# Optimization experiments

Hardware: AMD Instinct MI355X
Metric: run time of the kernel (lower is better)

Reference implementation:

```python
import jax, jax.numpy as jnp
import numpy as np

D_EMBED = 512
NUM_HEADS = 8
HEAD_DIM = D_EMBED // NUM_HEADS
D_FF = 2048
B, L = 2, 4096
LN_EPS = 1e-5


def _layernorm(x, g, b):
    mu = jnp.mean(x, axis=-1, keepdims=True)
    var = jnp.mean(jnp.square(x - mu), axis=-1, keepdims=True)
    return (x - mu) * jax.lax.rsqrt(var + LN_EPS) * g + b


def setup_inputs() -> dict:
    key = jax.random.key(0)
    ks = jax.random.split(key, 16)
    s = 0.02
    inp = {
        "x": jax.random.normal(ks[0], (B, L, D_EMBED), dtype=jnp.float32),
        "mask": jnp.ones((B, 1, 1, L), dtype=jnp.int32),
        # attention projections (stored [in, out] for x @ W)
        "Wq": jax.random.normal(ks[1], (D_EMBED, D_EMBED), dtype=jnp.float32) * s,
        "bq": jnp.zeros((D_EMBED,), dtype=jnp.float32),
        "Wk": jax.random.normal(ks[2], (D_EMBED, D_EMBED), dtype=jnp.float32) * s,
        "bk": jnp.zeros((D_EMBED,), dtype=jnp.float32),
        "Wv": jax.random.normal(ks[3], (D_EMBED, D_EMBED), dtype=jnp.float32) * s,
        "bv": jnp.zeros((D_EMBED,), dtype=jnp.float32),
        "Wo": jax.random.normal(ks[4], (D_EMBED, D_EMBED), dtype=jnp.float32) * s,
        "bo": jnp.zeros((D_EMBED,), dtype=jnp.float32),
        # layernorms
        "ln1_g": jnp.ones((D_EMBED,), dtype=jnp.float32),
        "ln1_b": jnp.zeros((D_EMBED,), dtype=jnp.float32),
        "ln2_g": jnp.ones((D_EMBED,), dtype=jnp.float32),
        "ln2_b": jnp.zeros((D_EMBED,), dtype=jnp.float32),
        # FFN
        "W1": jax.random.normal(ks[5], (D_EMBED, D_FF), dtype=jnp.float32) * s,
        "b1": jnp.zeros((D_FF,), dtype=jnp.float32),
        "W2": jax.random.normal(ks[6], (D_FF, D_EMBED), dtype=jnp.float32) * s,
        "b2": jnp.zeros((D_EMBED,), dtype=jnp.float32),
    }
    return inp


def reference(x, mask, Wq, bq, Wk, bk, Wv, bv, Wo, bo, ln1_g, ln1_b,
              W1, b1, W2, b2, ln2_g, ln2_b):
    Bx, Lx, _ = x.shape
    # projections -> [B, H, L, Dh]
    def split_heads(t):
        return t.reshape(Bx, Lx, NUM_HEADS, HEAD_DIM).transpose(0, 2, 1, 3)
    q = split_heads(x @ Wq + bq)
    k = split_heads(x @ Wk + bk)
    v = split_heads(x @ Wv + bv)
    scores = jnp.einsum("bhqd,bhkd->bhqk", q, k) / jnp.sqrt(
        jnp.asarray(HEAD_DIM, dtype=x.dtype))
    scores = jnp.where(mask == 0, jnp.asarray(-1e9, dtype=x.dtype), scores)
    attn = jax.nn.softmax(scores, axis=-1)
    ctx = jnp.einsum("bhqk,bhkd->bhqd", attn, v)
    ctx = ctx.transpose(0, 2, 1, 3).reshape(Bx, Lx, D_EMBED)
    attn_out = ctx @ Wo + bo

    h = _layernorm(x + attn_out, ln1_g, ln1_b)
    ff = (jax.nn.gelu(h @ W1 + b1, approximate=False)) @ W2 + b2
    return _layernorm(h + ff, ln2_g, ln2_b)
```

## Files before the change

kernel.cpp:

```cpp
#include <hip/hip_runtime.h>
#include <hip/hip_bf16.h>
#include <math.h>

#define D_EMBED 512
#define NUM_HEADS 8
#define HEAD_DIM 64
#define D_FF 2048
#define BATCH 2
#define SEQ 4096
#define M_ROWS (BATCH*SEQ)
#define QSCALE 0.18033688011112042f

typedef __attribute__((ext_vector_type(8))) short short8;
typedef __attribute__((ext_vector_type(4))) short short4_t;
typedef __attribute__((ext_vector_type(4))) float f32x4;

#if __has_builtin(__builtin_amdgcn_mfma_f32_16x16x16bf16_1k)
#define MFMA_K16(a,b,c) __builtin_amdgcn_mfma_f32_16x16x16bf16_1k(a,b,c,0,0,0)
#elif __has_builtin(__builtin_amdgcn_mfma_f32_16x16x16_bf16)
#define MFMA_K16(a,b,c) __builtin_amdgcn_mfma_f32_16x16x16_bf16(a,b,c,0,0,0)
#else
#define MFMA_K16(a,b,c) (c)
#endif

#if __has_builtin(__builtin_amdgcn_exp2f)
#define EXP2(x) __builtin_amdgcn_exp2f(x)
#else
#define EXP2(x) exp2f(x)
#endif

__device__ inline unsigned short f2b(float f) {
    union { float f; unsigned u; } v; v.f = f;
    unsigned r = v.u + 0x7fffu + ((v.u >> 16) & 1u);
    return (unsigned short)(r >> 16);
}

__device__ inline float b2f(short s) {
    union { unsigned u; float f; } v;
    v.u = ((unsigned)(unsigned short)s) << 16;
    return v.f;
}

__device__ inline short4_t pk4(float p0, float p1, float p2, float p3) {
    union { __hip_bfloat162 h2[2]; short4_t s4; } u;
    u.h2[0] = __float22bfloat162_rn(make_float2(p0, p1));
    u.h2[1] = __float22bfloat162_rn(make_float2(p2, p3));
    return u.s4;
}

__device__ inline void gl2lds16(const void* g, void* l) {
    __builtin_amdgcn_global_load_lds(
        (const __attribute__((address_space(1))) unsigned int*)g,
        (__attribute__((address_space(3))) unsigned int*)l, 16, 0, 0);
}

template<int EPI>
__global__ __launch_bounds__(256) void gemm_bt(
    const unsigned short* __restrict__ A, const unsigned short* __restrict__ BT,
    const float* __restrict__ bias, void* __restrict__ Cout,
    int M, int N, int K)
{
    __shared__ __align__(16) unsigned short As[128*32];
    __shared__ __align__(16) unsigned short Bs[128*32];
    const int tid  = threadIdx.x;
    const int wave = tid >> 6, lane = tid & 63;
    const int wy = wave >> 1, wx = wave & 1;
    const int quad = lane >> 4, m16 = lane & 15;
    const int row0 = blockIdx.y * 128, n0 = blockIdx.x * 128;
    const int rdoff = (quad ^ ((m16 >> 1) & 3)) * 8;

    f32x4 acc[4][4];
#pragma unroll
    for (int i = 0; i < 4; i++)
#pragma unroll
        for (int j = 0; j < 4; j++) acc[i][j] = (f32x4){0.f,0.f,0.f,0.f};

    const int kIters = K >> 5;
    for (int kt = 0; kt < kIters; ++kt) {
        const int k0 = kt << 5;
#pragma unroll
        for (int it = 0; it < 2; ++it) {
            int g  = it*256 + tid;
            int r  = g >> 2;
            int c8 = (((g & 3) ^ ((g >> 3) & 3)) << 3);
            gl2lds16(A  + (size_t)(row0 + r)*K + k0 + c8, &As[(size_t)(it*256 + wave*64)*8]);
            gl2lds16(BT + (size_t)(n0  + r)*K + k0 + c8, &Bs[(size_t)(it*256 + wave*64)*8]);
        }
        __syncthreads();
        short8 a[4], b[4];
#pragma unroll
        for (int i = 0; i < 4; i++) a[i] = *(const short8*)&As[(wy*64 + i*16 + m16)*32 + rdoff];
#pragma unroll
        for (int j = 0; j < 4; j++) b[j] = *(const short8*)&Bs[(wx*64 + j*16 + m16)*32 + rdoff];
#pragma unroll
        for (int i = 0; i < 4; i++)
#pragma unroll
            for (int j = 0; j < 4; j++)
                acc[i][j] = __builtin_amdgcn_mfma_f32_16x16x32_bf16(a[i], b[j], acc[i][j], 0, 0, 0);
        __syncthreads();
    }

#pragma unroll
    for (int j = 0; j < 4; j++) {
        int col = n0 + wx*64 + j*16 + m16;
        float bj = bias[col];
#pragma unroll
        for (int i = 0; i < 4; i++) {
            int rbase = row0 + wy*64 + i*16 + quad*4;
#pragma unroll
            for (int r = 0; r < 4; r++) {
                float v = acc[i][j][r] + bj;
                size_t idx = (size_t)(rbase + r)*N + col;
                if (EPI == 0) {
                    ((unsigned short*)Cout)[idx] = f2b(v);
                } else {
                    float gv = 0.5f * v * (1.0f + erff(v * 0.70710678118654752f));
                    ((unsigned short*)Cout)[idx] = f2b(gv);
                }
            }
        }
    }
}

__global__ __launch_bounds__(256) void gemm_qkv(
    const unsigned short* __restrict__ A, const unsigned short* __restrict__ BT,
    const float* __restrict__ bias,
    unsigned short* __restrict__ Qp, unsigned short* __restrict__ Kp,
    unsigned short* __restrict__ Vp)
{
    const int K = 512;
    __shared__ __align__(16) unsigned short As[128*32];
    __shared__ __align__(16) unsigned short Bs[128*32];
    const int tid  = threadIdx.x;
    const int wave = tid >> 6, lane = tid & 63;
    const int wy = wave >> 1, wx = wave & 1;
    const int quad = lane >> 4, m16 = lane & 15;
    const int row0 = blockIdx.y * 128, n0 = blockIdx.x * 128;
    const int rdoff = (quad ^ ((m16 >> 1) & 3)) * 8;
    const int region = n0 >> 9;

    f32x4 acc[4][4];
#pragma unroll
    for (int i = 0; i < 4; i++)
#pragma unroll
        for (int j = 0; j < 4; j++) acc[i][j] = (f32x4){0.f,0.f,0.f,0.f};

    for (int kt = 0; kt < 16; ++kt) {
        const int k0 = kt << 5;
#pragma unroll
        for (int it = 0; it < 2; ++it) {
            int g  = it*256 + tid;
            int r  = g >> 2;
            int c8 = (((g & 3) ^ ((g >> 3) & 3)) << 3);
            gl2lds16(A  + (size_t)(row0 + r)*K + k0 + c8, &As[(size_t)(it*256 + wave*64)*8]);
            gl2lds16(BT + (size_t)(n0  + r)*K + k0 + c8, &Bs[(size_t)(it*256 + wave*64)*8]);
        }
        __syncthreads();
        short8 a[4], b[4];
#pragma unroll
        for (int i = 0; i < 4; i++) a[i] = *(const short8*)&As[(wy*64 + i*16 + m16)*32 + rdoff];
#pragma unroll
        for (int j = 0; j < 4; j++) b[j] = *(const short8*)&Bs[(wx*64 + j*16 + m16)*32 + rdoff];
#pragma unroll
        for (int i = 0; i < 4; i++)
#pragma unroll
            for (int j = 0; j < 4; j++)
                acc[i][j] = __builtin_amdgcn_mfma_f32_16x16x32_bf16(a[i], b[j], acc[i][j], 0, 0, 0);
        __syncthreads();
    }

    const float sc = (region == 0) ? QSCALE : 1.0f;
#pragma unroll
    for (int j = 0; j < 4; j++) {
        int col = n0 + wx*64 + j*16 + m16;
        float bj = bias[col];
        int cc = col & 511, h = cc >> 6, d = cc & 63;
#pragma unroll
        for (int i = 0; i < 4; i++) {
            int rbase = row0 + wy*64 + i*16 + quad*4;
#pragma unroll
            for (int r = 0; r < 4; r++) {
                float v = (acc[i][j][r] + bj) * sc;
                int row = rbase + r;
                int b = row >> 12, l = row & 4095;
                size_t bh = (size_t)(b*8 + h);
                if (region == 0) {
                    Qp[(bh*SEQ + l)*64 + d] = f2b(v);
                } else if (region == 1) {
                    Kp[(bh*SEQ + l)*64 + d] = f2b(v);
                } else {
                    int kt = l >> 7, kk = l & 127;
                    int qr = (kk >> 2) & 3, fi = (kk >> 4)*4 + (kk & 3);
                    Vp[((((bh*32 + kt)*4 + qr)*64 + d)*32) + fi] = f2b(v);
                }
            }
        }
    }
}

__global__ __launch_bounds__(256) void gemm_bt64(
    const unsigned short* __restrict__ A, const unsigned short* __restrict__ BT,
    const float* __restrict__ bias, unsigned short* __restrict__ Cout,
    int M, int N, int K)
{
    __shared__ __align__(16) unsigned short As[64*32];
    __shared__ __align__(16) unsigned short Bs[128*32];
    const int tid  = threadIdx.x;
    const int wave = tid >> 6, lane = tid & 63;
    const int wy = wave >> 1, wx = wave & 1;
    const int quad = lane >> 4, m16 = lane & 15;
    const int row0 = blockIdx.y * 64, n0 = blockIdx.x * 128;
    const int rdoff = (quad ^ ((m16 >> 1) & 3)) * 8;

    f32x4 acc[2][4];
#pragma unroll
    for (int i = 0; i < 2; i++)
#pragma unroll
        for (int j = 0; j < 4; j++) acc[i][j] = (f32x4){0.f,0.f,0.f,0.f};

    const int kIters = K >> 5;
    for (int kt = 0; kt < kIters; ++kt) {
        const int k0 = kt << 5;
        {
            int r = tid >> 2;
            int c8 = (((tid & 3) ^ ((tid >> 3) & 3)) << 3);
            gl2lds16(A + (size_t)(row0 + r)*K + k0 + c8, &As[(size_t)(wave*64)*8]);
        }
#pragma unroll
        for (int it = 0; it < 2; ++it) {
            int g  = it*256 + tid;
            int r  = g >> 2;
            int c8 = (((g & 3) ^ ((g >> 3) & 3)) << 3);
            gl2lds16(BT + (size_t)(n0 + r)*K + k0 + c8, &Bs[(size_t)(it*256 + wave*64)*8]);
        }
        __syncthreads();
        short8 a[2], b[4];
#pragma unroll
        for (int i = 0; i < 2; i++) a[i] = *(const short8*)&As[(wy*32 + i*16 + m16)*32 + rdoff];
#pragma unroll
        for (int j = 0; j < 4; j++) b[j] = *(const short8*)&Bs[(wx*64 + j*16 + m16)*32 + rdoff];
#pragma unroll
        for (int i = 0; i < 2; i++)
#pragma unroll
            for (int j = 0; j < 4; j++)
                acc[i][j] = __builtin_amdgcn_mfma_f32_16x16x32_bf16(a[i], b[j], acc[i][j], 0, 0, 0);
        __syncthreads();
    }

#pragma unroll
    for (int j = 0; j < 4; j++) {
        int col = n0 + wx*64 + j*16 + m16;
        float bj = bias[col];
#pragma unroll
        for (int i = 0; i < 2; i++) {
            int rbase = row0 + wy*32 + i*16 + quad*4;
#pragma unroll
            for (int r = 0; r < 4; r++) {
                float v = acc[i][j][r] + bj;
                Cout[(size_t)(rbase + r)*N + col] = f2b(v);
            }
        }
    }
}

__global__ __launch_bounds__(256) void prep(
    const float* __restrict__ Wq, const float* __restrict__ Wk,
    const float* __restrict__ Wv, const float* __restrict__ Wo,
    const float* __restrict__ W1, const float* __restrict__ W2,
    const float* __restrict__ bq, const float* __restrict__ bk,
    const float* __restrict__ bv, const int* __restrict__ mask,
    unsigned short* __restrict__ WqkvT, unsigned short* __restrict__ WoT,
    unsigned short* __restrict__ W1T, unsigned short* __restrict__ W2T,
    float* __restrict__ bqkv, int* __restrict__ mflag, unsigned* __restrict__ kmax2)
{
    const int id = blockIdx.x, t = threadIdx.x;
    if (id == 3072) {
        if (t < 64) {
            const int* m = mask + t*128;
            int all = 1;
            for (int i = 0; i < 128; i += 4) {
                int4 v = *(const int4*)(m + i);
                all &= (v.x && v.y && v.z && v.w) ? 1 : 0;
            }
            mflag[t] = all;
        }
        if (t < 16) kmax2[t] = 0u;
        for (int i = t; i < 1536; i += 256)
            bqkv[i] = (i < 512) ? bq[i] : ((i < 1024) ? bk[i-512] : bv[i-1024]);
        return;
    }
    __shared__ float tt[32][33];
    const float* W; unsigned short* WT; int K, N, bx, by;
    if (id < 256)       { W = Wq; WT = WqkvT;            K = 512;  N = 512;  bx = id & 15;  by = id >> 4; }
    else if (id < 512)  { int l = id - 256;  W = Wk; WT = WqkvT + 512*512;  K = 512;  N = 512;  bx = l & 15; by = l >> 4; }
    else if (id < 768)  { int l = id - 512;  W = Wv; WT = WqkvT + 1024*512; K = 512;  N = 512;  bx = l & 15; by = l >> 4; }
    else if (id < 1024) { int l = id - 768;  W = Wo; WT = WoT;              K = 512;  N = 512;  bx = l & 15; by = l >> 4; }
    else if (id < 2048) { int l = id - 1024; W = W1; WT = W1T;              K = 512;  N = 2048; bx = l & 63; by = l >> 6; }
    else                { int l = id - 2048; W = W2; WT = W2T;              K = 2048; N = 512;  bx = l & 15; by = l >> 4; }
    const int n0 = bx*32, k0 = by*32;
    const int x = t & 31, y = t >> 5;
#pragma unroll
    for (int yy = y; yy < 32; yy += 8) tt[yy][x] = W[(size_t)(k0+yy)*N + n0 + x];
    __syncthreads();
#pragma unroll
    for (int yy = y; yy < 32; yy += 8) WT[(size_t)(n0+yy)*K + k0 + x] = f2b(tt[x][yy]);
}

__global__ __launch_bounds__(256) void kmax_k(
    const unsigned short* __restrict__ Kp, unsigned* __restrict__ kmax2)
{
    const int bh = blockIdx.x, t = threadIdx.x;
    const int row = blockIdx.y*256 + t;
    const unsigned short* kp = Kp + ((size_t)bh*SEQ + row)*64;
    float s = 0.f;
#pragma unroll
    for (int c = 0; c < 8; ++c) {
        short8 v = *(const short8*)(kp + c*8);
#pragma unroll
        for (int j = 0; j < 8; ++j) { float f = b2f(v[j]); s += f*f; }
    }
#pragma unroll
    for (int off = 32; off >= 1; off >>= 1)
        s = fmaxf(s, __shfl_xor(s, off, 64));
    if ((t & 63) == 0) atomicMax(&kmax2[bh], __float_as_uint(s));
}

__global__ __launch_bounds__(256) void flash_attn(
    const unsigned short* __restrict__ Qp, const unsigned short* __restrict__ Kp,
    const unsigned short* __restrict__ Vp, const int* __restrict__ mask,
    const int* __restrict__ flags, const unsigned* __restrict__ kmax2,
    unsigned short* __restrict__ O)
{
    __shared__ __align__(16) unsigned short Ks[2][128*32];
    __shared__ __align__(16) unsigned short Vs[4][64*32];
    const int tid = threadIdx.x, wave = tid >> 6, lane = tid & 63;
    const int quad = lane >> 4, m16 = lane & 15;
    const int bh = blockIdx.y, b = bh >> 3, h = bh & 7;
    const int qbase = blockIdx.x * 64 + wave * 16;
    const int fsw = (m16 >> 1) & 3;
    const int koff = (quad ^ fsw) * 8;

    const unsigned short* Qb = Qp + (size_t)bh*SEQ*64;
    const unsigned short* Kb = Kp + (size_t)bh*SEQ*64;
    const unsigned short* Vb = Vp + (size_t)bh*32*4*64*32;
    const int* mbase = mask + b*SEQ;
    const int* fbase = flags + b*(SEQ/128);

    short8 qf[2];
    {
        const unsigned short* qp = Qb + (size_t)(qbase + m16)*64 + quad*8;
        qf[0] = *(const short8*)qp;
        qf[1] = *(const short8*)(qp + 32);
    }
    float qn2 = 0.f;
#pragma unroll
    for (int j = 0; j < 8; ++j) {
        float f0 = b2f(qf[0][j]), f1 = b2f(qf[1][j]);
        qn2 += f0*f0 + f1*f1;
    }
    qn2 += __shfl_xor(qn2, 16, 64);
    qn2 += __shfl_xor(qn2, 32, 64);
    const float M = sqrtf(qn2 * __uint_as_float(kmax2[bh]));
    const f32x4 cinit = (f32x4){-M, -M, -M, -M};

    f32x4 accO[4];
#pragma unroll
    for (int dj = 0; dj < 4; dj++) accO[dj] = (f32x4){0.f,0.f,0.f,0.f};
    float rs = 0.f;

    for (int kt = 0; kt < SEQ/128; ++kt) {
        const int key0 = kt * 128;
        const int allones = fbase[kt];
        __syncthreads();
#pragma unroll
        for (int it = 0; it < 2; ++it) {
            int g = it*256 + tid;
            int r = g >> 2;
            int c8 = (((g & 3) ^ ((g >> 3) & 3)) << 3);
            gl2lds16(Kb + (size_t)(key0 + r)*64 + c8,      &Ks[0][(it*256 + wave*64)*8]);
            gl2lds16(Kb + (size_t)(key0 + r)*64 + 32 + c8, &Ks[1][(it*256 + wave*64)*8]);
        }
        {
            int d = wave*16 + (lane >> 2), ch = lane & 3;
            int c8 = (ch ^ ((d >> 1) & 3)) * 8;
#pragma unroll
            for (int qr = 0; qr < 4; ++qr)
                gl2lds16(Vb + (((size_t)kt*4 + qr)*64 + d)*32 + c8,
                         &Vs[qr][wave*64*8]);
        }
        __syncthreads();

        short4_t pb[8];
#pragma unroll
        for (int nj = 0; nj < 8; ++nj) {
            short8 k0 = *(const short8*)&Ks[0][(nj*16 + m16)*32 + koff];
            short8 k1 = *(const short8*)&Ks[1][(nj*16 + m16)*32 + koff];
            f32x4 c = cinit;
            c = __builtin_amdgcn_mfma_f32_16x16x32_bf16(k0, qf[0], c, 0, 0, 0);
            c = __builtin_amdgcn_mfma_f32_16x16x32_bf16(k1, qf[1], c, 0, 0, 0);
            if (!allones) {
                int4 mv = *(const int4*)(mbase + key0 + nj*16 + quad*4);
                c[0] = mv.x ? c[0] : -1e9f;
                c[1] = mv.y ? c[1] : -1e9f;
                c[2] = mv.z ? c[2] : -1e9f;
                c[3] = mv.w ? c[3] : -1e9f;
            }
            float p0 = EXP2(c[0]);
            float p1 = EXP2(c[1]);
            float p2 = EXP2(c[2]);
            float p3 = EXP2(c[3]);
            rs += (p0 + p1) + (p2 + p3);
            pb[nj] = pk4(p0, p1, p2, p3);
        }

#pragma unroll
        for (int l = 0; l < 4; ++l) {
#pragma unroll
            for (int dj = 0; dj < 4; ++dj) {
                const unsigned short* vrow = &Vs[quad][(dj*16 + m16)*32 + ((l ^ fsw) * 8)];
                short4_t vlo = *(const short4_t*)vrow;
                short4_t vhi = *(const short4_t*)(vrow + 4);
                accO[dj] = MFMA_K16(vlo, pb[2*l],     accO[dj]);
                accO[dj] = MFMA_K16(vhi, pb[2*l + 1], accO[dj]);
            }
        }
    }

    rs += __shfl_xor(rs, 16, 64);
    rs += __shfl_xor(rs, 32, 64);
    float rl = 1.0f / rs;
#pragma unroll
    for (int dj = 0; dj < 4; ++dj) {
        short4_t o = pk4(accO[dj][0]*rl, accO[dj][1]*rl,
                         accO[dj][2]*rl, accO[dj][3]*rl);
        *(short4_t*)&O[(size_t)(b*SEQ + qbase + m16)*D_EMBED
                       + h*HEAD_DIM + dj*16 + quad*4] = o;
    }
}

__global__ __launch_bounds__(256) void ln_res1(
    const float* __restrict__ A, const unsigned short* __restrict__ Bv,
    const float* __restrict__ g, const float* __restrict__ be,
    unsigned short* __restrict__ Yb)
{
    const int wave = threadIdx.x >> 6, lane = threadIdx.x & 63;
    const int row = blockIdx.x * 4 + wave;
    const float* ap = A + (size_t)row*512 + lane*8;
    short8 bv = *(const short8*)(Bv + (size_t)row*512 + lane*8);
    float v[8]; float s = 0.f;
#pragma unroll
    for (int j = 0; j < 8; j++) { v[j] = ap[j] + b2f(bv[j]); s += v[j]; }
#pragma unroll
    for (int off = 32; off >= 1; off >>= 1) s += __shfl_xor(s, off, 64);
    float mu = s * (1.f/512.f);
    float q = 0.f;
#pragma unroll
    for (int j = 0; j < 8; j++) { v[j] -= mu; q += v[j]*v[j]; }
#pragma unroll
    for (int off = 32; off >= 1; off >>= 1) q += __shfl_xor(q, off, 64);
    float rstd = rsqrtf(q * (1.f/512.f) + 1e-5f);
#pragma unroll
    for (int j = 0; j < 8; j++) {
        float y = v[j]*rstd*g[lane*8+j] + be[lane*8+j];
        Yb[(size_t)row*512 + lane*8 + j] = f2b(y);
    }
}

__global__ __launch_bounds__(256) void ln_res2(
    const unsigned short* __restrict__ A, const unsigned short* __restrict__ Bv,
    const float* __restrict__ g, const float* __restrict__ be,
    float* __restrict__ Yf)
{
    const int wave = threadIdx.x >> 6, lane = threadIdx.x & 63;
    const int row = blockIdx.x * 4 + wave;
    short8 av = *(const short8*)(A  + (size_t)row*512 + lane*8);
    short8 bv = *(const short8*)(Bv + (size_t)row*512 + lane*8);
    float v[8]; float s = 0.f;
#pragma unroll
    for (int j = 0; j < 8; j++) { v[j] = b2f(av[j]) + b2f(bv[j]); s += v[j]; }
#pragma unroll
    for (int off = 32; off >= 1; off >>= 1) s += __shfl_xor(s, off, 64);
    float mu = s * (1.f/512.f);
    float q = 0.f;
#pragma unroll
    for (int j = 0; j < 8; j++) { v[j] -= mu; q += v[j]*v[j]; }
#pragma unroll
    for (int off = 32; off >= 1; off >>= 1) q += __shfl_xor(q, off, 64);
    float rstd = rsqrtf(q * (1.f/512.f) + 1e-5f);
#pragma unroll
    for (int j = 0; j < 8; j++) {
        float y = v[j]*rstd*g[lane*8+j] + be[lane*8+j];
        Yf[(size_t)row*512 + lane*8 + j] = y;
    }
}

__global__ __launch_bounds__(256) void cvt_f32_bf16(
    const float* __restrict__ X, unsigned short* __restrict__ Y, int n)
{
    int idx = (blockIdx.x * 256 + threadIdx.x) * 4;
    if (idx < n) {
        float4 v = *(const float4*)(X + idx);
        Y[idx+0] = f2b(v.x); Y[idx+1] = f2b(v.y);
        Y[idx+2] = f2b(v.z); Y[idx+3] = f2b(v.w);
    }
}

extern "C" void kernel_launch(void* const* d_in, const int* in_sizes, int n_in,
                              void* d_out, int out_size, void* d_ws, size_t ws_size,
                              hipStream_t stream)
{
    const float* x    = (const float*)d_in[0];
    const int*   mask = (const int*)  d_in[1];
    const float* Wq = (const float*)d_in[2];  const float* bq = (const float*)d_in[3];
    const float* Wk = (const float*)d_in[4];  const float* bk = (const float*)d_in[5];
    const float* Wv = (const float*)d_in[6];  const float* bv = (const float*)d_in[7];
    const float* Wo = (const float*)d_in[8];  const float* bo = (const float*)d_in[9];
    const float* ln1g = (const float*)d_in[10]; const float* ln1b = (const float*)d_in[11];
    const float* ln2g = (const float*)d_in[12]; const float* ln2b = (const float*)d_in[13];
    const float* W1 = (const float*)d_in[14]; const float* b1 = (const float*)d_in[15];
    const float* W2 = (const float*)d_in[16]; const float* b2 = (const float*)d_in[17];
    float* out = (float*)d_out;

    char* ws = (char*)d_ws;
    const size_t MB = 1024*1024;
    unsigned short* xb    = (unsigned short*)(ws + 0);
    unsigned short* WqkvT = (unsigned short*)(ws + 8*MB);
    unsigned short* W1T   = (unsigned short*)(ws + 10*MB);
    unsigned short* W2T   = (unsigned short*)(ws + 12*MB);
    unsigned short* WoT   = (unsigned short*)(ws + 14*MB);
    float*          bqkv  = (float*)(ws + 14*MB + 512*1024);
    int*            mflag = (int*)(ws + 14*MB + 768*1024);
    unsigned*       kmaxb = (unsigned*)(ws + 14*MB + 772*1024);
    unsigned short* Qp    = (unsigned short*)(ws + 15*MB);
    unsigned short* Kp    = (unsigned short*)(ws + 23*MB);
    unsigned short* Vp    = (unsigned short*)(ws + 31*MB);
    unsigned short* ctx   = (unsigned short*)(ws + 39*MB);
    unsigned short* atfb  = (unsigned short*)(ws + 47*MB);
    unsigned short* hb    = (unsigned short*)(ws + 0);
    unsigned short* Gb    = (unsigned short*)(ws + 15*MB);
    unsigned short* ffb   = (unsigned short*)(ws + 47*MB);

    cvt_f32_bf16<<<4096, 256, 0, stream>>>(x, xb, M_ROWS*D_EMBED);
    prep<<<3073, 256, 0, stream>>>(Wq, Wk, Wv, Wo, W1, W2, bq, bk, bv, mask,
                                   WqkvT, WoT, W1T, W2T, bqkv, mflag, kmaxb);

    gemm_qkv<<<dim3(12,64), 256, 0, stream>>>(xb, WqkvT, bqkv, Qp, Kp, Vp);

    kmax_k<<<dim3(16,16), 256, 0, stream>>>(Kp, kmaxb);
    flash_attn<<<dim3(SEQ/64, 16), 256, 0, stream>>>(Qp, Kp, Vp, mask, mflag, kmaxb, ctx);

    gemm_bt64<<<dim3(4,128), 256, 0, stream>>>(ctx, WoT, bo, atfb, M_ROWS, 512, 512);
    ln_res1<<<M_ROWS/4, 256, 0, stream>>>(x, atfb, ln1g, ln1b, hb);

    gemm_bt<2><<<dim3(16,64), 256, 0, stream>>>(hb, W1T, b1, Gb, M_ROWS, D_FF, 512);
    gemm_bt64<<<dim3(4,128), 256, 0, stream>>>(Gb, W2T, b2, ffb, M_ROWS, 512, D_FF);
    ln_res2<<<M_ROWS/4, 256, 0, stream>>>(hb, ffb, ln2g, ln2b, out);
}
```

Baseline: 381.2 us.

## Double GEMM K-tile to 64 with 8-way XOR swizzle; fuse x conversion into prep

Measured after the change: 382.3 us. No clear change (+0.3%).

```diff
diff --git a/kernel.cpp b/kernel.cpp
--- a/kernel.cpp
+++ b/kernel.cpp
@@ -54,20 +54,21 @@
         (__attribute__((address_space(3))) unsigned int*)l, 16, 0, 0);
 }
 
+
 template<int EPI>
 __global__ __launch_bounds__(256) void gemm_bt(
     const unsigned short* __restrict__ A, const unsigned short* __restrict__ BT,
     const float* __restrict__ bias, void* __restrict__ Cout,
     int M, int N, int K)
 {
-    __shared__ __align__(16) unsigned short As[128*32];
-    __shared__ __align__(16) unsigned short Bs[128*32];
+    __shared__ __align__(16) unsigned short As[128*64];
+    __shared__ __align__(16) unsigned short Bs[128*64];
     const int tid  = threadIdx.x;
     const int wave = tid >> 6, lane = tid & 63;
     const int wy = wave >> 1, wx = wave & 1;
     const int quad = lane >> 4, m16 = lane & 15;
     const int row0 = blockIdx.y * 128, n0 = blockIdx.x * 128;
-    const int rdoff = (quad ^ ((m16 >> 1) & 3)) * 8;
+    const int rsw = m16 & 7;
 
     f32x4 acc[4][4];
 #pragma unroll
@@ -75,28 +76,33 @@
 #pragma unroll
         for (int j = 0; j < 4; j++) acc[i][j] = (f32x4){0.f,0.f,0.f,0.f};
 
-    const int kIters = K >> 5;
+    const int kIters = K >> 6;
     for (int kt = 0; kt < kIters; ++kt) {
-        const int k0 = kt << 5;
-#pragma unroll
-        for (int it = 0; it < 2; ++it) {
+        const int k0 = kt << 6;
+#pragma unroll
+        for (int it = 0; it < 4; ++it) {
             int g  = it*256 + tid;
-            int r  = g >> 2;
-            int c8 = (((g & 3) ^ ((g >> 3) & 3)) << 3);
+            int r  = g >> 3;
+            int c8 = (((g & 7) ^ (r & 7)) << 3);
             gl2lds16(A  + (size_t)(row0 + r)*K + k0 + c8, &As[(size_t)(it*256 + wave*64)*8]);
             gl2lds16(BT + (size_t)(n0  + r)*K + k0 + c8, &Bs[(size_t)(it*256 + wave*64)*8]);
         }
         __syncthreads();
-        short8 a[4], b[4];
-#pragma unroll
-        for (int i = 0; i < 4; i++) a[i] = *(const short8*)&As[(wy*64 + i*16 + m16)*32 + rdoff];
-#pragma unroll
-        for (int j = 0; j < 4; j++) b[j] = *(const short8*)&Bs[(wx*64 + j*16 + m16)*32 + rdoff];
-#pragma unroll
-        for (int i = 0; i < 4; i++)
+#pragma unroll
+        for (int s = 0; s < 2; ++s) {
+            short8 a[4], b[4];
+#pragma unroll
+            for (int i = 0; i < 4; i++)
+                a[i] = *(const short8*)&As[(wy*64 + i*16 + m16)*64 + ((((s<<2)|quad) ^ rsw)*8)];
 #pragma unroll
             for (int j = 0; j < 4; j++)
-                acc[i][j] = __builtin_amdgcn_mfma_f32_16x16x32_bf16(a[i], b[j], acc[i][j], 0, 0, 0);
+                b[j] = *(const short8*)&Bs[(wx*64 + j*16 + m16)*64 + ((((s<<2)|quad) ^ rsw)*8)];
+#pragma unroll
+            for (int i = 0; i < 4; i++)
+#pragma unroll
+                for (int j = 0; j < 4; j++)
+                    acc[i][j] = __builtin_amdgcn_mfma_f32_16x16x32_bf16(a[i], b[j], acc[i][j], 0, 0, 0);
+        }
         __syncthreads();
     }
 
@@ -129,14 +135,14 @@
     unsigned short* __restrict__ Vp)
 {
     const int K = 512;
-    __shared__ __align__(16) unsigned short As[128*32];
-    __shared__ __align__(16) unsigned short Bs[128*32];
+    __shared__ __align__(16) unsigned short As[128*64];
+    __shared__ __align__(16) unsigned short Bs[128*64];
     const int tid  = threadIdx.x;
     const int wave = tid >> 6, lane = tid & 63;
     const int wy = wave >> 1, wx = wave & 1;
     const int quad = lane >> 4, m16 = lane & 15;
     const int row0 = blockIdx.y * 128, n0 = blockIdx.x * 128;
-    const int rdoff = (quad ^ ((m16 >> 1) & 3)) * 8;
+    const int rsw = m16 & 7;
     const int region = n0 >> 9;
 
     f32x4 acc[4][4];
@@ -145,27 +151,32 @@
 #pragma unroll
         for (int j = 0; j < 4; j++) acc[i][j] = (f32x4){0.f,0.f,0.f,0.f};
 
-    for (int kt = 0; kt < 16; ++kt) {
-        const int k0 = kt << 5;
-#pragma unroll
-        for (int it = 0; it < 2; ++it) {
+    for (int kt = 0; kt < 8; ++kt) {
+        const int k0 = kt << 6;
+#pragma unroll
+        for (int it = 0; it < 4; ++it) {
             int g  = it*256 + tid;
-            int r  = g >> 2;
-            int c8 = (((g & 3) ^ ((g >> 3) & 3)) << 3);
+            int r  = g >> 3;
+            int c8 = (((g & 7) ^ (r & 7)) << 3);
             gl2lds16(A  + (size_t)(row0 + r)*K + k0 + c8, &As[(size_t)(it*256 + wave*64)*8]);
             gl2lds16(BT + (size_t)(n0  + r)*K + k0 + c8, &Bs[(size_t)(it*256 + wave*64)*8]);
         }
         __syncthreads();
-        short8 a[4], b[4];
-#pragma unroll
-        for (int i = 0; i < 4; i++) a[i] = *(const short8*)&As[(wy*64 + i*16 + m16)*32 + rdoff];
-#pragma unroll
-        for (int j = 0; j < 4; j++) b[j] = *(const short8*)&Bs[(wx*64 + j*16 + m16)*32 + rdoff];
-#pragma unroll
-        for (int i = 0; i < 4; i++)
+#pragma unroll
+        for (int s = 0; s < 2; ++s) {
+            short8 a[4], b[4];
+#pragma unroll
+            for (int i = 0; i < 4; i++)
+                a[i] = *(const short8*)&As[(wy*64 + i*16 + m16)*64 + ((((s<<2)|quad) ^ rsw)*8)];
 #pragma unroll
             for (int j = 0; j < 4; j++)
-                acc[i][j] = __builtin_amdgcn_mfma_f32_16x16x32_bf16(a[i], b[j], acc[i][j], 0, 0, 0);
+                b[j] = *(const short8*)&Bs[(wx*64 + j*16 + m16)*64 + ((((s<<2)|quad) ^ rsw)*8)];
+#pragma unroll
+            for (int i = 0; i < 4; i++)
+#pragma unroll
+                for (int j = 0; j < 4; j++)
+                    acc[i][j] = __builtin_amdgcn_mfma_f32_16x16x32_bf16(a[i], b[j], acc[i][j], 0, 0, 0);
+        }
         __syncthreads();
     }
 
@@ -203,14 +214,14 @@
     const float* __restrict__ bias, unsigned short* __restrict__ Cout,
     int M, int N, int K)
 {
-    __shared__ __align__(16) unsigned short As[64*32];
-    __shared__ __align__(16) unsigned short Bs[128*32];
+    __shared__ __align__(16) unsigned short As[64*64];
+    __shared__ __align__(16) unsigned short Bs[128*64];
     const int tid  = threadIdx.x;
     const int wave = tid >> 6, lane = tid & 63;
     const int wy = wave >> 1, wx = wave & 1;
     const int quad = lane >> 4, m16 = lane & 15;
     const int row0 = blockIdx.y * 64, n0 = blockIdx.x * 128;
-    const int rdoff = (quad ^ ((m16 >> 1) & 3)) * 8;
+    const int rsw = m16 & 7;
 
     f32x4 acc[2][4];
 #pragma unroll
@@ -218,32 +229,39 @@
 #pragma unroll
         for (int j = 0; j < 4; j++) acc[i][j] = (f32x4){0.f,0.f,0.f,0.f};
 
-    const int kIters = K >> 5;
+    const int kIters = K >> 6;
     for (int kt = 0; kt < kIters; ++kt) {
-        const int k0 = kt << 5;
-        {
-            int r = tid >> 2;
-            int c8 = (((tid & 3) ^ ((tid >> 3) & 3)) << 3);
-            gl2lds16(A + (size_t)(row0 + r)*K + k0 + c8, &As[(size_t)(wave*64)*8]);
-        }
+        const int k0 = kt << 6;
 #pragma unroll
         for (int it = 0; it < 2; ++it) {
             int g  = it*256 + tid;
-            int r  = g >> 2;
-            int c8 = (((g & 3) ^ ((g >> 3) & 3)) << 3);
+            int r  = g >> 3;
+            int c8 = (((g & 7) ^ (r & 7)) << 3);
+            gl2lds16(A + (size_t)(row0 + r)*K + k0 + c8, &As[(size_t)(it*256 + wave*64)*8]);
+        }
+#pragma unroll
+        for (int it = 0; it < 4; ++it) {
+            int g  = it*256 + tid;
+            int r  = g >> 3;
+            int c8 = (((g & 7) ^ (r & 7)) << 3);
             gl2lds16(BT + (size_t)(n0 + r)*K + k0 + c8, &Bs[(size_t)(it*256 + wave*64)*8]);
         }
         __syncthreads();
-        short8 a[2], b[4];
-#pragma unroll
-        for (int i = 0; i < 2; i++) a[i] = *(const short8*)&As[(wy*32 + i*16 + m16)*32 + rdoff];
-#pragma unroll
-        for (int j = 0; j < 4; j++) b[j] = *(const short8*)&Bs[(wx*64 + j*16 + m16)*32 + rdoff];
-#pragma unroll
-        for (int i = 0; i < 2; i++)
+#pragma unroll
+        for (int s = 0; s < 2; ++s) {
+            short8 a[2], b[4];
+#pragma unroll
+            for (int i = 0; i < 2; i++)
+                a[i] = *(const short8*)&As[(wy*32 + i*16 + m16)*64 + ((((s<<2)|quad) ^ rsw)*8)];
 #pragma unroll
             for (int j = 0; j < 4; j++)
-                acc[i][j] = __builtin_amdgcn_mfma_f32_16x16x32_bf16(a[i], b[j], acc[i][j], 0, 0, 0);
+                b[j] = *(const short8*)&Bs[(wx*64 + j*16 + m16)*64 + ((((s<<2)|quad) ^ rsw)*8)];
+#pragma unroll
+            for (int i = 0; i < 2; i++)
+#pragma unroll
+                for (int j = 0; j < 4; j++)
+                    acc[i][j] = __builtin_amdgcn_mfma_f32_16x16x32_bf16(a[i], b[j], acc[i][j], 0, 0, 0);
+        }
         __syncthreads();
     }
 
@@ -269,11 +287,20 @@
     const float* __restrict__ W1, const float* __restrict__ W2,
     const float* __restrict__ bq, const float* __restrict__ bk,
     const float* __restrict__ bv, const int* __restrict__ mask,
+    const float* __restrict__ x,
     unsigned short* __restrict__ WqkvT, unsigned short* __restrict__ WoT,
     unsigned short* __restrict__ W1T, unsigned short* __restrict__ W2T,
-    float* __restrict__ bqkv, int* __restrict__ mflag, unsigned* __restrict__ kmax2)
+    float* __restrict__ bqkv, int* __restrict__ mflag, unsigned* __restrict__ kmax2,
+    unsigned short* __restrict__ xb)
 {
     const int id = blockIdx.x, t = threadIdx.x;
+    if (id >= 3073) {
+        int idx = (id - 3073)*1024 + t*4;
+        float4 v = *(const float4*)(x + idx);
+        xb[idx+0] = f2b(v.x); xb[idx+1] = f2b(v.y);
+        xb[idx+2] = f2b(v.z); xb[idx+3] = f2b(v.w);
+        return;
+    }
     if (id == 3072) {
         if (t < 64) {
             const int* m = mask + t*128;
@@ -298,12 +325,12 @@
     else if (id < 2048) { int l = id - 1024; W = W1; WT = W1T;              K = 512;  N = 2048; bx = l & 63; by = l >> 6; }
     else                { int l = id - 2048; W = W2; WT = W2T;              K = 2048; N = 512;  bx = l & 15; by = l >> 4; }
     const int n0 = bx*32, k0 = by*32;
-    const int x = t & 31, y = t >> 5;
-#pragma unroll
-    for (int yy = y; yy < 32; yy += 8) tt[yy][x] = W[(size_t)(k0+yy)*N + n0 + x];
+    const int x2 = t & 31, y2 = t >> 5;
+#pragma unroll
+    for (int yy = y2; yy < 32; yy += 8) tt[yy][x2] = W[(size_t)(k0+yy)*N + n0 + x2];
     __syncthreads();
 #pragma unroll
-    for (int yy = y; yy < 32; yy += 8) WT[(size_t)(n0+yy)*K + k0 + x] = f2b(tt[x][yy]);
+    for (int yy = y2; yy < 32; yy += 8) WT[(size_t)(n0+yy)*K + k0 + x2] = f2b(tt[x2][yy]);
 }
 
 __global__ __launch_bounds__(256) void kmax_k(
@@ -494,17 +521,6 @@
     }
 }
 
-__global__ __launch_bounds__(256) void cvt_f32_bf16(
-    const float* __restrict__ X, unsigned short* __restrict__ Y, int n)
-{
-    int idx = (blockIdx.x * 256 + threadIdx.x) * 4;
-    if (idx < n) {
-        float4 v = *(const float4*)(X + idx);
-        Y[idx+0] = f2b(v.x); Y[idx+1] = f2b(v.y);
-        Y[idx+2] = f2b(v.z); Y[idx+3] = f2b(v.w);
-    }
-}
-
 extern "C" void kernel_launch(void* const* d_in, const int* in_sizes, int n_in,
                               void* d_out, int out_size, void* d_ws, size_t ws_size,
                               hipStream_t stream)
@@ -540,9 +556,9 @@
     unsigned short* Gb    = (unsigned short*)(ws + 15*MB);
     unsigned short* ffb   = (unsigned short*)(ws + 47*MB);
 
-    cvt_f32_bf16<<<4096, 256, 0, stream>>>(x, xb, M_ROWS*D_EMBED);
-    prep<<<3073, 256, 0, stream>>>(Wq, Wk, Wv, Wo, W1, W2, bq, bk, bv, mask,
-                                   WqkvT, WoT, W1T, W2T, bqkv, mflag, kmaxb);
+    prep<<<3073 + 4096, 256, 0, stream>>>(Wq, Wk, Wv, Wo, W1, W2, bq, bk, bv,
+                                          mask, x, WqkvT, WoT, W1T, W2T,
+                                          bqkv, mflag, kmaxb, xb);
 
     gemm_qkv<<<dim3(12,64), 256, 0, stream>>>(xb, WqkvT, bqkv, Qp, Kp, Vp);
 
```
